# Performance work log

Hardware: AMD Instinct MI355X
Metric: run time of the kernel (lower is better)

## Reference

```python
import jax, jax.numpy as jnp
import numpy as np

N, D, S, C, H = 65536, 512, 32, 64, 64  # batch, input_size, n_subnets, cols/subnet, hidden
GROUP = 32  # columns per predictor group


def _build_col_ids():
    # 16 groups of 32 cols; interactions = (i,i+1) and (i,i+2) mod 16
    pairs = [(i, (i + 1) % 16) for i in range(16)] + [(i, (i + 2) % 16) for i in range(16)]
    ids = np.array([np.concatenate([np.arange(a * GROUP, (a + 1) * GROUP),
                                    np.arange(b * GROUP, (b + 1) * GROUP)])
                    for a, b in pairs], dtype=np.int32)  # [S, C]
    return jnp.asarray(ids)


def setup_inputs() -> dict:
    key = jax.random.key(0)
    ks = jax.random.split(key, 7)
    scale = 0.05  # keep log_rate inside clamp range most of the time
    return {
        "x": jax.random.normal(ks[0], (N, D), jnp.float32),
        "skip_w": jax.random.normal(ks[1], (D,), jnp.float32) * scale,
        "skip_b": jax.random.normal(ks[2], (1,), jnp.float32) * scale,
        "W1": jax.random.normal(ks[3], (S, C, H), jnp.float32) * scale,
        "b1": jax.random.normal(ks[4], (S, H), jnp.float32) * scale,
        "W2": jax.random.normal(ks[5], (S, H), jnp.float32) * scale,
        "b2": jax.random.normal(ks[6], (S,), jnp.float32) * scale,
        "col_ids": _build_col_ids(),
    }


def reference(x, skip_w, skip_b, W1, b1, W2, b2, col_ids):
    # skip: Linear(D,1) then squeeze -> [N]
    log_rate = x @ skip_w + skip_b[0]
    # fused gather + batched tiny MLP over all S subnets
    xg = x[:, col_ids]                                  # [N, S, C]
    h = jax.nn.relu(jnp.einsum('nsc,sch->nsh', xg, W1) + b1)  # [N, S, H]
    out = jnp.einsum('nsh,sh->ns', h, W2) + b2          # [N, S]
    log_rate = log_rate + out.sum(axis=-1)
    return jnp.clip(log_rate, -20.0, 20.0)
```

## Files before the change

kernel.cpp:

```cpp
#include <hip/hip_runtime.h>

#define NROWS 65536
#define DCOLS 512

typedef float  f32x4  __attribute__((ext_vector_type(4)));
typedef __bf16 bf16x8 __attribute__((ext_vector_type(8)));

__device__ __forceinline__ unsigned short f2bf(float f) {
    unsigned int u = __builtin_bit_cast(unsigned int, f);
    u += 0x7fffu + ((u >> 16) & 1u);
    return (unsigned short)(u >> 16);
}

__global__ void pack_kernel(const float* __restrict__ W1,
                            const float* __restrict__ b1,
                            const float* __restrict__ W2,
                            unsigned short* __restrict__ w1p,
                            float2* __restrict__ pk) {
    int idx  = blockIdx.x * 256 + threadIdx.x;
    int j    = idx & 7;
    int lane = (idx >> 3) & 63;
    int f    = (idx >> 9) & 7;
    int s    = idx >> 12;
    int kt = f >> 2, nt = f & 3;
    int c = kt * 32 + (lane >> 4) * 8 + j;
    int h = nt * 16 + (lane & 15);
    w1p[idx] = f2bf(W1[(s * 64 + c) * 64 + h]);
    if (idx < 2048) pk[idx] = make_float2(b1[idx], W2[idx]);
}

__launch_bounds__(256, 2)
__global__ void fused_kernel(const float* __restrict__ x,
                             const float* __restrict__ skip_w,
                             const float* __restrict__ skip_b,
                             const float* __restrict__ b2,
                             const unsigned short* __restrict__ w1p,
                             const float2* __restrict__ pk,
                             float* __restrict__ out) {
    __shared__ uint4 w1buf[2][512];

    const int tid  = threadIdx.x;
    const int wave = tid >> 6;
    const int lane = tid & 63;
    const int m    = lane & 15;
    const int q    = lane >> 4;
    const int row0 = blockIdx.x * 128 + wave * 32;

    uint4 afr[2][16];
    float sp[2] = {0.f, 0.f};
#pragma unroll
    for (int g = 0; g < 16; ++g) {
        const float4 sw0 = *(const float4*)(skip_w + g * 32 + q * 8);
        const float4 sw1 = *(const float4*)(skip_w + g * 32 + q * 8 + 4);
#pragma unroll
        for (int mt = 0; mt < 2; ++mt) {
            const float* xp = x + (long)(row0 + mt * 16 + m) * DCOLS + g * 32 + q * 8;
            const float4 a0 = *(const float4*)(xp);
            const float4 a1 = *(const float4*)(xp + 4);
            float s0 = fmaf(a0.x, sw0.x, fmaf(a0.y, sw0.y, fmaf(a0.z, sw0.z, a0.w * sw0.w)));
            float s1 = fmaf(a1.x, sw1.x, fmaf(a1.y, sw1.y, fmaf(a1.z, sw1.z, a1.w * sw1.w)));
            sp[mt] += s0 + s1;
            unsigned int u01 = (unsigned int)f2bf(a0.x) | ((unsigned int)f2bf(a0.y) << 16);
            unsigned int u23 = (unsigned int)f2bf(a0.z) | ((unsigned int)f2bf(a0.w) << 16);
            unsigned int u45 = (unsigned int)f2bf(a1.x) | ((unsigned int)f2bf(a1.y) << 16);
            unsigned int u67 = (unsigned int)f2bf(a1.z) | ((unsigned int)f2bf(a1.w) << 16);
            afr[mt][g] = make_uint4(u01, u23, u45, u67);
        }
    }
    float sf[2];
#pragma unroll
    for (int mt = 0; mt < 2; ++mt) {
        float v = sp[mt];
        v += __shfl_xor(v, 16);
        v += __shfl_xor(v, 32);
        sf[mt] = v;
    }

    float b2s = 0.f;
#pragma unroll
    for (int i = 0; i < 32; ++i) b2s += b2[i];
    const float sb0 = skip_b[0];

    const uint4* wp = (const uint4*)w1p;
    float part[2][4] = {{0.f,0.f,0.f,0.f},{0.f,0.f,0.f,0.f}};

    w1buf[0][tid]       = wp[tid];
    w1buf[0][tid + 256] = wp[tid + 256];
    __syncthreads();

#pragma unroll
    for (int s = 0; s < 32; ++s) {
        const int cb = s & 1, nb = cb ^ 1;
        if (s + 1 < 32) {
            w1buf[nb][tid]       = wp[(s + 1) * 512 + tid];
            w1buf[nb][tid + 256] = wp[(s + 1) * 512 + tid + 256];
        }
        const int ga = s & 15;
        const int gb = ((s & 15) + 1 + (s >> 4)) & 15;

        bf16x8 bfr[2][4];
#pragma unroll
        for (int kt = 0; kt < 2; ++kt)
#pragma unroll
            for (int nt = 0; nt < 4; ++nt)
                bfr[kt][nt] = __builtin_bit_cast(bf16x8, w1buf[cb][(kt * 4 + nt) * 64 + lane]);

        f32x4 acc[2][4];
#pragma unroll
        for (int mt = 0; mt < 2; ++mt) {
            const bf16x8 a0 = __builtin_bit_cast(bf16x8, afr[mt][ga]);
            const bf16x8 a1 = __builtin_bit_cast(bf16x8, afr[mt][gb]);
#pragma unroll
            for (int nt = 0; nt < 4; ++nt) {
                f32x4 z = {0.f, 0.f, 0.f, 0.f};
                acc[mt][nt] = __builtin_amdgcn_mfma_f32_16x16x32_bf16(a0, bfr[0][nt], z, 0, 0, 0);
                acc[mt][nt] = __builtin_amdgcn_mfma_f32_16x16x32_bf16(a1, bfr[1][nt], acc[mt][nt], 0, 0, 0);
            }
        }

#pragma unroll
        for (int nt = 0; nt < 4; ++nt) {
            const float2 bw = pk[s * 64 + nt * 16 + m];
#pragma unroll
            for (int mt = 0; mt < 2; ++mt)
#pragma unroll
                for (int r = 0; r < 4; ++r) {
                    float h = acc[mt][nt][r] + bw.x;
                    h = fmaxf(h, 0.f);
                    part[mt][r] = fmaf(h, bw.y, part[mt][r]);
                }
        }
        __syncthreads();
    }

#pragma unroll
    for (int mt = 0; mt < 2; ++mt)
#pragma unroll
        for (int r = 0; r < 4; ++r) {
            float v = part[mt][r];
            v += __shfl_xor(v, 1);
            v += __shfl_xor(v, 2);
            v += __shfl_xor(v, 4);
            v += __shfl_xor(v, 8);
            const float skipv = __shfl(sf[mt], q * 4 + r);
            float val = v + b2s + sb0 + skipv;
            val = fminf(fmaxf(val, -20.f), 20.f);
            if (m == 0) out[row0 + mt * 16 + q * 4 + r] = val;
        }
}

extern "C" void kernel_launch(void* const* d_in, const int* in_sizes, int n_in,
                              void* d_out, int out_size, void* d_ws, size_t ws_size,
                              hipStream_t stream) {
    const float* x      = (const float*)d_in[0];
    const float* skip_w = (const float*)d_in[1];
    const float* skip_b = (const float*)d_in[2];
    const float* W1     = (const float*)d_in[3];
    const float* b1     = (const float*)d_in[4];
    const float* W2     = (const float*)d_in[5];
    const float* b2     = (const float*)d_in[6];

    unsigned short* w1p = (unsigned short*)d_ws;
    float2* pk = (float2*)((char*)d_ws + 262144);

    pack_kernel<<<512, 256, 0, stream>>>(W1, b1, W2, w1p, pk);
    fused_kernel<<<NROWS / 128, 256, 0, stream>>>(x, skip_w, skip_b, b2, w1p, pk,
                                                  (float*)d_out);
}
```

Measured before the change: 225.4 us.

## Halve rows per wave, raise occupancy, and stream weights via global_load_lds

```diff
diff --git a/kernel.cpp b/kernel.cpp
--- a/kernel.cpp
+++ b/kernel.cpp
@@ -12,24 +12,29 @@
     return (unsigned short)(u >> 16);
 }
 
+#define GLOAD_LDS16(gp, lp)                                                   \
+    __builtin_amdgcn_global_load_lds(                                         \
+        (__attribute__((address_space(1))) void*)(gp),                        \
+        (__attribute__((address_space(3))) void*)(lp), 16, 0, 0)
+
 __global__ void pack_kernel(const float* __restrict__ W1,
                             const float* __restrict__ b1,
                             const float* __restrict__ W2,
                             unsigned short* __restrict__ w1p,
                             float2* __restrict__ pk) {
-    int idx  = blockIdx.x * 256 + threadIdx.x;
-    int j    = idx & 7;
-    int lane = (idx >> 3) & 63;
-    int f    = (idx >> 9) & 7;
-    int s    = idx >> 12;
-    int kt = f >> 2, nt = f & 3;
-    int c = kt * 32 + (lane >> 4) * 8 + j;
-    int h = nt * 16 + (lane & 15);
-    w1p[idx] = f2bf(W1[(s * 64 + c) * 64 + h]);
+    int idx = blockIdx.x * 256 + threadIdx.x;
+    int s = idx >> 12;
+    int c = (idx >> 6) & 63;
+    int h = idx & 63;
+    int kt = c >> 5, nt = h >> 4;
+    int lane = (((c & 31) >> 3) << 4) | (h & 15);
+    int j = c & 7;
+    int dst = (s << 12) | (((kt << 2) | nt) << 9) | (lane << 3) | j;
+    w1p[dst] = f2bf(W1[idx]);
     if (idx < 2048) pk[idx] = make_float2(b1[idx], W2[idx]);
 }
 
-__launch_bounds__(256, 2)
+__launch_bounds__(256, 4)
 __global__ void fused_kernel(const float* __restrict__ x,
                              const float* __restrict__ skip_w,
                              const float* __restrict__ skip_b,
@@ -44,109 +49,90 @@
     const int lane = tid & 63;
     const int m    = lane & 15;
     const int q    = lane >> 4;
-    const int row0 = blockIdx.x * 128 + wave * 32;
+    const int row0 = blockIdx.x * 64 + wave * 16;
 
-    uint4 afr[2][16];
-    float sp[2] = {0.f, 0.f};
+    const uint4* wp = (const uint4*)w1p;
+    GLOAD_LDS16(wp + tid,       &w1buf[0][wave * 64]);
+    GLOAD_LDS16(wp + 256 + tid, &w1buf[0][256 + wave * 64]);
+
+    uint4 afr[16];
+    float sp = 0.f;
+    const float* xbase  = x + (long)(row0 + m) * DCOLS + q * 8;
+    const float* swbase = skip_w + q * 8;
 #pragma unroll
     for (int g = 0; g < 16; ++g) {
-        const float4 sw0 = *(const float4*)(skip_w + g * 32 + q * 8);
-        const float4 sw1 = *(const float4*)(skip_w + g * 32 + q * 8 + 4);
-#pragma unroll
-        for (int mt = 0; mt < 2; ++mt) {
-            const float* xp = x + (long)(row0 + mt * 16 + m) * DCOLS + g * 32 + q * 8;
-            const float4 a0 = *(const float4*)(xp);
-            const float4 a1 = *(const float4*)(xp + 4);
-            float s0 = fmaf(a0.x, sw0.x, fmaf(a0.y, sw0.y, fmaf(a0.z, sw0.z, a0.w * sw0.w)));
-            float s1 = fmaf(a1.x, sw1.x, fmaf(a1.y, sw1.y, fmaf(a1.z, sw1.z, a1.w * sw1.w)));
-            sp[mt] += s0 + s1;
-            unsigned int u01 = (unsigned int)f2bf(a0.x) | ((unsigned int)f2bf(a0.y) << 16);
-            unsigned int u23 = (unsigned int)f2bf(a0.z) | ((unsigned int)f2bf(a0.w) << 16);
-            unsigned int u45 = (unsigned int)f2bf(a1.x) | ((unsigned int)f2bf(a1.y) << 16);
-            unsigned int u67 = (unsigned int)f2bf(a1.z) | ((unsigned int)f2bf(a1.w) << 16);
-            afr[mt][g] = make_uint4(u01, u23, u45, u67);
-        }
+        const float4 sw0 = *(const float4*)(swbase + g * 32);
+        const float4 sw1 = *(const float4*)(swbase + g * 32 + 4);
+        const float4 a0  = *(const float4*)(xbase + g * 32);
+        const float4 a1  = *(const float4*)(xbase + g * 32 + 4);
+        float s0 = fmaf(a0.x, sw0.x, fmaf(a0.y, sw0.y, fmaf(a0.z, sw0.z, a0.w * sw0.w)));
+        float s1 = fmaf(a1.x, sw1.x, fmaf(a1.y, sw1.y, fmaf(a1.z, sw1.z, a1.w * sw1.w)));
+        sp += s0 + s1;
+        unsigned int u01 = (unsigned int)f2bf(a0.x) | ((unsigned int)f2bf(a0.y) << 16);
+        unsigned int u23 = (unsigned int)f2bf(a0.z) | ((unsigned int)f2bf(a0.w) << 16);
+        unsigned int u45 = (unsigned int)f2bf(a1.x) | ((unsigned int)f2bf(a1.y) << 16);
+        unsigned int u67 = (unsigned int)f2bf(a1.z) | ((unsigned int)f2bf(a1.w) << 16);
+        afr[g] = make_uint4(u01, u23, u45, u67);
     }
-    float sf[2];
-#pragma unroll
-    for (int mt = 0; mt < 2; ++mt) {
-        float v = sp[mt];
-        v += __shfl_xor(v, 16);
-        v += __shfl_xor(v, 32);
-        sf[mt] = v;
-    }
+    float sv = sp;
+    sv += __shfl_xor(sv, 16);
+    sv += __shfl_xor(sv, 32);
+    const float sf = sv;
 
     float b2s = 0.f;
 #pragma unroll
     for (int i = 0; i < 32; ++i) b2s += b2[i];
     const float sb0 = skip_b[0];
 
-    const uint4* wp = (const uint4*)w1p;
-    float part[2][4] = {{0.f,0.f,0.f,0.f},{0.f,0.f,0.f,0.f}};
-
-    w1buf[0][tid]       = wp[tid];
-    w1buf[0][tid + 256] = wp[tid + 256];
+    float part[4] = {0.f, 0.f, 0.f, 0.f};
     __syncthreads();
 
 #pragma unroll
     for (int s = 0; s < 32; ++s) {
         const int cb = s & 1, nb = cb ^ 1;
         if (s + 1 < 32) {
-            w1buf[nb][tid]       = wp[(s + 1) * 512 + tid];
-            w1buf[nb][tid + 256] = wp[(s + 1) * 512 + tid + 256];
+            GLOAD_LDS16(wp + (s + 1) * 512 + tid,       &w1buf[nb][wave * 64]);
+            GLOAD_LDS16(wp + (s + 1) * 512 + 256 + tid, &w1buf[nb][256 + wave * 64]);
         }
         const int ga = s & 15;
-        const int gb = ((s & 15) + 1 + (s >> 4)) & 15;
+        const int gb = (ga + 1 + (s >> 4)) & 15;
+        const bf16x8 a0 = __builtin_bit_cast(bf16x8, afr[ga]);
+        const bf16x8 a1 = __builtin_bit_cast(bf16x8, afr[gb]);
 
-        bf16x8 bfr[2][4];
+        f32x4 acc[4];
 #pragma unroll
-        for (int kt = 0; kt < 2; ++kt)
-#pragma unroll
-            for (int nt = 0; nt < 4; ++nt)
-                bfr[kt][nt] = __builtin_bit_cast(bf16x8, w1buf[cb][(kt * 4 + nt) * 64 + lane]);
-
-        f32x4 acc[2][4];
-#pragma unroll
-        for (int mt = 0; mt < 2; ++mt) {
-            const bf16x8 a0 = __builtin_bit_cast(bf16x8, afr[mt][ga]);
-            const bf16x8 a1 = __builtin_bit_cast(bf16x8, afr[mt][gb]);
-#pragma unroll
-            for (int nt = 0; nt < 4; ++nt) {
-                f32x4 z = {0.f, 0.f, 0.f, 0.f};
-                acc[mt][nt] = __builtin_amdgcn_mfma_f32_16x16x32_bf16(a0, bfr[0][nt], z, 0, 0, 0);
-                acc[mt][nt] = __builtin_amdgcn_mfma_f32_16x16x32_bf16(a1, bfr[1][nt], acc[mt][nt], 0, 0, 0);
-            }
+        for (int nt = 0; nt < 4; ++nt) {
+            const bf16x8 b0 = __builtin_bit_cast(bf16x8, w1buf[cb][nt * 64 + lane]);
+            const bf16x8 b1v = __builtin_bit_cast(bf16x8, w1buf[cb][(4 + nt) * 64 + lane]);
+            f32x4 z = {0.f, 0.f, 0.f, 0.f};
+            f32x4 t = __builtin_amdgcn_mfma_f32_16x16x32_bf16(a0, b0, z, 0, 0, 0);
+            acc[nt] = __builtin_amdgcn_mfma_f32_16x16x32_bf16(a1, b1v, t, 0, 0, 0);
         }
 
 #pragma unroll
         for (int nt = 0; nt < 4; ++nt) {
             const float2 bw = pk[s * 64 + nt * 16 + m];
 #pragma unroll
-            for (int mt = 0; mt < 2; ++mt)
-#pragma unroll
-                for (int r = 0; r < 4; ++r) {
-                    float h = acc[mt][nt][r] + bw.x;
-                    h = fmaxf(h, 0.f);
-                    part[mt][r] = fmaf(h, bw.y, part[mt][r]);
-                }
+            for (int r = 0; r < 4; ++r) {
+                float hh = fmaxf(acc[nt][r] + bw.x, 0.f);
+                part[r] = fmaf(hh, bw.y, part[r]);
+            }
         }
         __syncthreads();
     }
 
 #pragma unroll
-    for (int mt = 0; mt < 2; ++mt)
-#pragma unroll
-        for (int r = 0; r < 4; ++r) {
-            float v = part[mt][r];
-            v += __shfl_xor(v, 1);
-            v += __shfl_xor(v, 2);
-            v += __shfl_xor(v, 4);
-            v += __shfl_xor(v, 8);
-            const float skipv = __shfl(sf[mt], q * 4 + r);
-            float val = v + b2s + sb0 + skipv;
-            val = fminf(fmaxf(val, -20.f), 20.f);
-            if (m == 0) out[row0 + mt * 16 + q * 4 + r] = val;
-        }
+    for (int r = 0; r < 4; ++r) {
+        float v = part[r];
+        v += __shfl_xor(v, 1);
+        v += __shfl_xor(v, 2);
+        v += __shfl_xor(v, 4);
+        v += __shfl_xor(v, 8);
+        const float skipv = __shfl(sf, q * 4 + r);
+        float val = v + b2s + sb0 + skipv;
+        val = fminf(fmaxf(val, -20.f), 20.f);
+        if (m == 0) out[row0 + q * 4 + r] = val;
+    }
 }
 
 extern "C" void kernel_launch(void* const* d_in, const int* in_sizes, int n_in,
@@ -164,6 +150,6 @@
     float2* pk = (float2*)((char*)d_ws + 262144);
 
     pack_kernel<<<512, 256, 0, stream>>>(W1, b1, W2, w1p, pk);
-    fused_kernel<<<NROWS / 128, 256, 0, stream>>>(x, skip_w, skip_b, b2, w1p, pk,
-                                                  (float*)d_out);
+    fused_kernel<<<NROWS / 64, 256, 0, stream>>>(x, skip_w, skip_b, b2, w1p, pk,
+                                                 (float*)d_out);
 }
```

New measurement: 244.2 us. 8.4% more time.

## Load packed W1 fragments directly into registers, drop LDS staging and block barriers

Applied to the files above, without the earlier changes.

```diff
diff --git a/kernel.cpp b/kernel.cpp
--- a/kernel.cpp
+++ b/kernel.cpp
@@ -17,19 +17,19 @@
                             const float* __restrict__ W2,
                             unsigned short* __restrict__ w1p,
                             float2* __restrict__ pk) {
-    int idx  = blockIdx.x * 256 + threadIdx.x;
-    int j    = idx & 7;
-    int lane = (idx >> 3) & 63;
-    int f    = (idx >> 9) & 7;
-    int s    = idx >> 12;
-    int kt = f >> 2, nt = f & 3;
-    int c = kt * 32 + (lane >> 4) * 8 + j;
-    int h = nt * 16 + (lane & 15);
-    w1p[idx] = f2bf(W1[(s * 64 + c) * 64 + h]);
+    int idx = blockIdx.x * 256 + threadIdx.x;
+    int s = idx >> 12;
+    int c = (idx >> 6) & 63;
+    int h = idx & 63;
+    int kt = c >> 5, nt = h >> 4;
+    int lane = (((c & 31) >> 3) << 4) | (h & 15);
+    int j = c & 7;
+    int dst = (s << 12) | (((kt << 2) | nt) << 9) | (lane << 3) | j;
+    w1p[dst] = f2bf(W1[idx]);
     if (idx < 2048) pk[idx] = make_float2(b1[idx], W2[idx]);
 }
 
-__launch_bounds__(256, 2)
+__launch_bounds__(64, 2)
 __global__ void fused_kernel(const float* __restrict__ x,
                              const float* __restrict__ skip_w,
                              const float* __restrict__ skip_b,
@@ -37,14 +37,10 @@
                              const unsigned short* __restrict__ w1p,
                              const float2* __restrict__ pk,
                              float* __restrict__ out) {
-    __shared__ uint4 w1buf[2][512];
-
-    const int tid  = threadIdx.x;
-    const int wave = tid >> 6;
-    const int lane = tid & 63;
+    const int lane = threadIdx.x;
     const int m    = lane & 15;
     const int q    = lane >> 4;
-    const int row0 = blockIdx.x * 128 + wave * 32;
+    const int row0 = blockIdx.x * 32;
 
     uint4 afr[2][16];
     float sp[2] = {0.f, 0.f};
@@ -81,29 +77,27 @@
     for (int i = 0; i < 32; ++i) b2s += b2[i];
     const float sb0 = skip_b[0];
 
-    const uint4* wp = (const uint4*)w1p;
+    const uint4* wl = (const uint4*)w1p + lane;
+
     float part[2][4] = {{0.f,0.f,0.f,0.f},{0.f,0.f,0.f,0.f}};
 
-    w1buf[0][tid]       = wp[tid];
-    w1buf[0][tid + 256] = wp[tid + 256];
-    __syncthreads();
+    uint4 braw[2][8];
+#pragma unroll
+    for (int f = 0; f < 8; ++f) braw[0][f] = wl[f * 64];
 
 #pragma unroll
     for (int s = 0; s < 32; ++s) {
         const int cb = s & 1, nb = cb ^ 1;
         if (s + 1 < 32) {
-            w1buf[nb][tid]       = wp[(s + 1) * 512 + tid];
-            w1buf[nb][tid + 256] = wp[(s + 1) * 512 + tid + 256];
+#pragma unroll
+            for (int f = 0; f < 8; ++f) braw[nb][f] = wl[(s + 1) * 512 + f * 64];
         }
+        float2 bw[4];
+#pragma unroll
+        for (int nt = 0; nt < 4; ++nt) bw[nt] = pk[s * 64 + nt * 16 + m];
+
         const int ga = s & 15;
-        const int gb = ((s & 15) + 1 + (s >> 4)) & 15;
-
-        bf16x8 bfr[2][4];
-#pragma unroll
-        for (int kt = 0; kt < 2; ++kt)
-#pragma unroll
-            for (int nt = 0; nt < 4; ++nt)
-                bfr[kt][nt] = __builtin_bit_cast(bf16x8, w1buf[cb][(kt * 4 + nt) * 64 + lane]);
+        const int gb = (ga + 1 + (s >> 4)) & 15;
 
         f32x4 acc[2][4];
 #pragma unroll
@@ -113,24 +107,22 @@
 #pragma unroll
             for (int nt = 0; nt < 4; ++nt) {
                 f32x4 z = {0.f, 0.f, 0.f, 0.f};
-                acc[mt][nt] = __builtin_amdgcn_mfma_f32_16x16x32_bf16(a0, bfr[0][nt], z, 0, 0, 0);
-                acc[mt][nt] = __builtin_amdgcn_mfma_f32_16x16x32_bf16(a1, bfr[1][nt], acc[mt][nt], 0, 0, 0);
+                f32x4 t = __builtin_amdgcn_mfma_f32_16x16x32_bf16(
+                              a0, __builtin_bit_cast(bf16x8, braw[cb][nt]), z, 0, 0, 0);
+                acc[mt][nt] = __builtin_amdgcn_mfma_f32_16x16x32_bf16(
+                              a1, __builtin_bit_cast(bf16x8, braw[cb][4 + nt]), t, 0, 0, 0);
             }
         }
 
 #pragma unroll
-        for (int nt = 0; nt < 4; ++nt) {
-            const float2 bw = pk[s * 64 + nt * 16 + m];
+        for (int nt = 0; nt < 4; ++nt)
 #pragma unroll
             for (int mt = 0; mt < 2; ++mt)
 #pragma unroll
                 for (int r = 0; r < 4; ++r) {
-                    float h = acc[mt][nt][r] + bw.x;
-                    h = fmaxf(h, 0.f);
-                    part[mt][r] = fmaf(h, bw.y, part[mt][r]);
+                    float hh = fmaxf(acc[mt][nt][r] + bw[nt].x, 0.f);
+                    part[mt][r] = fmaf(hh, bw[nt].y, part[mt][r]);
                 }
-        }
-        __syncthreads();
     }
 
 #pragma unroll
@@ -164,6 +156,6 @@
     float2* pk = (float2*)((char*)d_ws + 262144);
 
     pack_kernel<<<512, 256, 0, stream>>>(W1, b1, W2, w1p, pk);
-    fused_kernel<<<NROWS / 128, 256, 0, stream>>>(x, skip_w, skip_b, b2, w1p, pk,
-                                                  (float*)d_out);
+    fused_kernel<<<NROWS / 32, 64, 0, stream>>>(x, skip_w, skip_b, b2, w1p, pk,
+                                                (float*)d_out);
 }
```

Result: slower. 897.7 us (+298.3%).

## Split x preprocessing into a separate bf16 conversion and skip-dot kernel

Applied to the files above, without the earlier changes.

```diff
diff --git a/kernel.cpp b/kernel.cpp
--- a/kernel.cpp
+++ b/kernel.cpp
@@ -10,6 +10,64 @@
     unsigned int u = __builtin_bit_cast(unsigned int, f);
     u += 0x7fffu + ((u >> 16) & 1u);
     return (unsigned short)(u >> 16);
+}
+
+__device__ __forceinline__ void pack_body(int idx,
+                                          const float* __restrict__ W1,
+                                          const float* __restrict__ b1,
+                                          const float* __restrict__ W2,
+                                          unsigned short* __restrict__ w1p,
+                                          float2* __restrict__ pk) {
+    int s = idx >> 12;
+    int c = (idx >> 6) & 63;
+    int h = idx & 63;
+    int kt = c >> 5, nt = h >> 4;
+    int lane = (((c & 31) >> 3) << 4) | (h & 15);
+    int j = c & 7;
+    int dst = (s << 12) | (((kt << 2) | nt) << 9) | (lane << 3) | j;
+    w1p[dst] = f2bf(W1[idx]);
+    if (idx < 2048) pk[idx] = make_float2(b1[idx], W2[idx]);
+}
+
+__global__ void xprep_pack_kernel(const float* __restrict__ x,
+                                  const float* __restrict__ skip_w,
+                                  const float* __restrict__ W1,
+                                  const float* __restrict__ b1,
+                                  const float* __restrict__ W2,
+                                  uint4* __restrict__ xp,
+                                  float* __restrict__ logr,
+                                  unsigned short* __restrict__ w1p,
+                                  float2* __restrict__ pk) {
+    if (blockIdx.x >= 2048) {
+        pack_body((blockIdx.x - 2048) * 256 + threadIdx.x, W1, b1, W2, w1p, pk);
+        return;
+    }
+    const int lane = threadIdx.x & 63;
+    const int wid  = blockIdx.x * 4 + (threadIdx.x >> 6);
+    const float4 sw0 = *(const float4*)(skip_w + lane * 8);
+    const float4 sw1 = *(const float4*)(skip_w + lane * 8 + 4);
+#pragma unroll 2
+    for (int i = 0; i < 8; ++i) {
+        const int r = wid * 8 + i;
+        const float* xr = x + (long)r * DCOLS + lane * 8;
+        const float4 a0 = *(const float4*)(xr);
+        const float4 a1 = *(const float4*)(xr + 4);
+        float d = fmaf(a0.x, sw0.x, fmaf(a0.y, sw0.y, fmaf(a0.z, sw0.z, a0.w * sw0.w)));
+        d = fmaf(a1.x, sw1.x, fmaf(a1.y, sw1.y, fmaf(a1.z, sw1.z, fmaf(a1.w, sw1.w, d))));
+        d += __shfl_xor(d, 1);
+        d += __shfl_xor(d, 2);
+        d += __shfl_xor(d, 4);
+        d += __shfl_xor(d, 8);
+        d += __shfl_xor(d, 16);
+        d += __shfl_xor(d, 32);
+        if (lane == 0) logr[r] = d;
+        uint4 u;
+        u.x = (unsigned int)f2bf(a0.x) | ((unsigned int)f2bf(a0.y) << 16);
+        u.y = (unsigned int)f2bf(a0.z) | ((unsigned int)f2bf(a0.w) << 16);
+        u.z = (unsigned int)f2bf(a1.x) | ((unsigned int)f2bf(a1.y) << 16);
+        u.w = (unsigned int)f2bf(a1.z) | ((unsigned int)f2bf(a1.w) << 16);
+        xp[(long)r * 64 + lane] = u;
+    }
 }
 
 __global__ void pack_kernel(const float* __restrict__ W1,
@@ -17,21 +75,24 @@
                             const float* __restrict__ W2,
                             unsigned short* __restrict__ w1p,
                             float2* __restrict__ pk) {
-    int idx  = blockIdx.x * 256 + threadIdx.x;
-    int j    = idx & 7;
-    int lane = (idx >> 3) & 63;
-    int f    = (idx >> 9) & 7;
-    int s    = idx >> 12;
-    int kt = f >> 2, nt = f & 3;
-    int c = kt * 32 + (lane >> 4) * 8 + j;
-    int h = nt * 16 + (lane & 15);
-    w1p[idx] = f2bf(W1[(s * 64 + c) * 64 + h]);
-    if (idx < 2048) pk[idx] = make_float2(b1[idx], W2[idx]);
+    pack_body(blockIdx.x * 256 + threadIdx.x, W1, b1, W2, w1p, pk);
+}
+
+__global__ void prefetch_kernel(const float* __restrict__ x) {
+    const int tid = blockIdx.x * 256 + threadIdx.x;
+    float4 a = make_float4(0.f, 0.f, 0.f, 0.f);
+    const float4* xv = (const float4*)x;
+#pragma unroll
+    for (int i = 0; i < 16; ++i) {
+        float4 v = xv[(long)i * 524288 + tid];
+        a.x += v.x; a.y += v.y; a.z += v.z; a.w += v.w;
+    }
+    asm volatile("" :: "v"(a.x), "v"(a.y), "v"(a.z), "v"(a.w));
 }
 
 __launch_bounds__(256, 2)
-__global__ void fused_kernel(const float* __restrict__ x,
-                             const float* __restrict__ skip_w,
+__global__ void fused_packed(const uint4* __restrict__ xp,
+                             const float* __restrict__ logr,
                              const float* __restrict__ skip_b,
                              const float* __restrict__ b2,
                              const unsigned short* __restrict__ w1p,
@@ -47,34 +108,15 @@
     const int row0 = blockIdx.x * 128 + wave * 32;
 
     uint4 afr[2][16];
-    float sp[2] = {0.f, 0.f};
-#pragma unroll
-    for (int g = 0; g < 16; ++g) {
-        const float4 sw0 = *(const float4*)(skip_w + g * 32 + q * 8);
-        const float4 sw1 = *(const float4*)(skip_w + g * 32 + q * 8 + 4);
-#pragma unroll
-        for (int mt = 0; mt < 2; ++mt) {
-            const float* xp = x + (long)(row0 + mt * 16 + m) * DCOLS + g * 32 + q * 8;
-            const float4 a0 = *(const float4*)(xp);
-            const float4 a1 = *(const float4*)(xp + 4);
-            float s0 = fmaf(a0.x, sw0.x, fmaf(a0.y, sw0.y, fmaf(a0.z, sw0.z, a0.w * sw0.w)));
-            float s1 = fmaf(a1.x, sw1.x, fmaf(a1.y, sw1.y, fmaf(a1.z, sw1.z, a1.w * sw1.w)));
-            sp[mt] += s0 + s1;
-            unsigned int u01 = (unsigned int)f2bf(a0.x) | ((unsigned int)f2bf(a0.y) << 16);
-            unsigned int u23 = (unsigned int)f2bf(a0.z) | ((unsigned int)f2bf(a0.w) << 16);
-            unsigned int u45 = (unsigned int)f2bf(a1.x) | ((unsigned int)f2bf(a1.y) << 16);
-            unsigned int u67 = (unsigned int)f2bf(a1.z) | ((unsigned int)f2bf(a1.w) << 16);
-            afr[mt][g] = make_uint4(u01, u23, u45, u67);
-        }
+#pragma unroll
+    for (int mt = 0; mt < 2; ++mt) {
+        const uint4* xrow = xp + (long)(row0 + mt * 16 + m) * 64 + q;
+#pragma unroll
+        for (int g = 0; g < 16; ++g) afr[mt][g] = xrow[g * 4];
     }
     float sf[2];
 #pragma unroll
-    for (int mt = 0; mt < 2; ++mt) {
-        float v = sp[mt];
-        v += __shfl_xor(v, 16);
-        v += __shfl_xor(v, 32);
-        sf[mt] = v;
-    }
+    for (int mt = 0; mt < 2; ++mt) sf[mt] = logr[row0 + mt * 16 + m];
 
     float b2s = 0.f;
 #pragma unroll
@@ -149,6 +191,126 @@
         }
 }
 
+__launch_bounds__(256, 2)
+__global__ void fused_kernel(const float* __restrict__ x,
+                             const float* __restrict__ skip_w,
+                             const float* __restrict__ skip_b,
+                             const float* __restrict__ b2,
+                             const unsigned short* __restrict__ w1p,
+                             const float2* __restrict__ pk,
+                             float* __restrict__ out) {
+    __shared__ uint4 w1buf[2][512];
+
+    const int tid  = threadIdx.x;
+    const int wave = tid >> 6;
+    const int lane = tid & 63;
+    const int m    = lane & 15;
+    const int q    = lane >> 4;
+    const int row0 = blockIdx.x * 128 + wave * 32;
+
+    uint4 afr[2][16];
+    float sp[2] = {0.f, 0.f};
+#pragma unroll
+    for (int g = 0; g < 16; ++g) {
+        const float4 sw0 = *(const float4*)(skip_w + g * 32 + q * 8);
+        const float4 sw1 = *(const float4*)(skip_w + g * 32 + q * 8 + 4);
+#pragma unroll
+        for (int mt = 0; mt < 2; ++mt) {
+            const float* xpr = x + (long)(row0 + mt * 16 + m) * DCOLS + g * 32 + q * 8;
+            const float4 a0 = *(const float4*)(xpr);
+            const float4 a1 = *(const float4*)(xpr + 4);
+            float s0 = fmaf(a0.x, sw0.x, fmaf(a0.y, sw0.y, fmaf(a0.z, sw0.z, a0.w * sw0.w)));
+            float s1 = fmaf(a1.x, sw1.x, fmaf(a1.y, sw1.y, fmaf(a1.z, sw1.z, a1.w * sw1.w)));
+            sp[mt] += s0 + s1;
+            unsigned int u01 = (unsigned int)f2bf(a0.x) | ((unsigned int)f2bf(a0.y) << 16);
+            unsigned int u23 = (unsigned int)f2bf(a0.z) | ((unsigned int)f2bf(a0.w) << 16);
+            unsigned int u45 = (unsigned int)f2bf(a1.x) | ((unsigned int)f2bf(a1.y) << 16);
+            unsigned int u67 = (unsigned int)f2bf(a1.z) | ((unsigned int)f2bf(a1.w) << 16);
+            afr[mt][g] = make_uint4(u01, u23, u45, u67);
+        }
+    }
+    float sf[2];
+#pragma unroll
+    for (int mt = 0; mt < 2; ++mt) {
+        float v = sp[mt];
+        v += __shfl_xor(v, 16);
+        v += __shfl_xor(v, 32);
+        sf[mt] = v;
+    }
+
+    float b2s = 0.f;
+#pragma unroll
+    for (int i = 0; i < 32; ++i) b2s += b2[i];
+    const float sb0 = skip_b[0];
+
+    const uint4* wp = (const uint4*)w1p;
+    float part[2][4] = {{0.f,0.f,0.f,0.f},{0.f,0.f,0.f,0.f}};
+
+    w1buf[0][tid]       = wp[tid];
+    w1buf[0][tid + 256] = wp[tid + 256];
+    __syncthreads();
+
+#pragma unroll
+    for (int s = 0; s < 32; ++s) {
+        const int cb = s & 1, nb = cb ^ 1;
+        if (s + 1 < 32) {
+            w1buf[nb][tid]       = wp[(s + 1) * 512 + tid];
+            w1buf[nb][tid + 256] = wp[(s + 1) * 512 + tid + 256];
+        }
+        const int ga = s & 15;
+        const int gb = ((s & 15) + 1 + (s >> 4)) & 15;
+
+        bf16x8 bfr[2][4];
+#pragma unroll
+        for (int kt = 0; kt < 2; ++kt)
+#pragma unroll
+            for (int nt = 0; nt < 4; ++nt)
+                bfr[kt][nt] = __builtin_bit_cast(bf16x8, w1buf[cb][(kt * 4 + nt) * 64 + lane]);
+
+        f32x4 acc[2][4];
+#pragma unroll
+        for (int mt = 0; mt < 2; ++mt) {
+            const bf16x8 a0 = __builtin_bit_cast(bf16x8, afr[mt][ga]);
+            const bf16x8 a1 = __builtin_bit_cast(bf16x8, afr[mt][gb]);
+#pragma unroll
+            for (int nt = 0; nt < 4; ++nt) {
+                f32x4 z = {0.f, 0.f, 0.f, 0.f};
+                acc[mt][nt] = __builtin_amdgcn_mfma_f32_16x16x32_bf16(a0, bfr[0][nt], z, 0, 0, 0);
+                acc[mt][nt] = __builtin_amdgcn_mfma_f32_16x16x32_bf16(a1, bfr[1][nt], acc[mt][nt], 0, 0, 0);
+            }
+        }
+
+#pragma unroll
+        for (int nt = 0; nt < 4; ++nt) {
+            const float2 bw = pk[s * 64 + nt * 16 + m];
+#pragma unroll
+            for (int mt = 0; mt < 2; ++mt)
+#pragma unroll
+                for (int r = 0; r < 4; ++r) {
+                    float h = acc[mt][nt][r] + bw.x;
+                    h = fmaxf(h, 0.f);
+                    part[mt][r] = fmaf(h, bw.y, part[mt][r]);
+                }
+        }
+        __syncthreads();
+    }
+
+#pragma unroll
+    for (int mt = 0; mt < 2; ++mt)
+#pragma unroll
+        for (int r = 0; r < 4; ++r) {
+            float v = part[mt][r];
+            v += __shfl_xor(v, 1);
+            v += __shfl_xor(v, 2);
+            v += __shfl_xor(v, 4);
+            v += __shfl_xor(v, 8);
+            const float skipv = __shfl(sf[mt], q * 4 + r);
+            float val = v + b2s + sb0 + skipv;
+            val = fminf(fmaxf(val, -20.f), 20.f);
+            if (m == 0) out[row0 + mt * 16 + q * 4 + r] = val;
+        }
+}
+
 extern "C" void kernel_launch(void* const* d_in, const int* in_sizes, int n_in,
                               void* d_out, int out_size, void* d_ws, size_t ws_size,
                               hipStream_t stream) {
@@ -161,9 +323,20 @@
     const float* b2     = (const float*)d_in[6];
 
     unsigned short* w1p = (unsigned short*)d_ws;
-    float2* pk = (float2*)((char*)d_ws + 262144);
-
-    pack_kernel<<<512, 256, 0, stream>>>(W1, b1, W2, w1p, pk);
-    fused_kernel<<<NROWS / 128, 256, 0, stream>>>(x, skip_w, skip_b, b2, w1p, pk,
-                                                  (float*)d_out);
-}
+    float2* pk   = (float2*)((char*)d_ws + 262144);
+    float*  logr = (float*)((char*)d_ws + 278528);
+    uint4*  xp   = (uint4*)((char*)d_ws + 540672);
+    const size_t need = 540672 + (size_t)NROWS * DCOLS * 2;
+
+    if (ws_size >= need) {
+        xprep_pack_kernel<<<2560, 256, 0, stream>>>(x, skip_w, W1, b1, W2,
+                                                    xp, logr, w1p, pk);
+        fused_packed<<<NROWS / 128, 256, 0, stream>>>(xp, logr, skip_b, b2,
+                                                      w1p, pk, (float*)d_out);
+    } else {
+        pack_kernel<<<512, 256, 0, stream>>>(W1, b1, W2, w1p, pk);
+        prefetch_kernel<<<2048, 256, 0, stream>>>(x);
+        fused_kernel<<<NROWS / 128, 256, 0, stream>>>(x, skip_w, skip_b, b2,
+                                                      w1p, pk, (float*)d_out);
+    }
+}
```

New measurement: 245.3 us. 1.09x slower.
